# Kernel optimization log

Measured on AMD Instinct MI355X. Metric: run time of the kernel, lower is better.

## Reference

```python
import jax, jax.numpy as jnp
import numpy as np

EPS = 1e-4          # scn.BatchNormLeakyReLU default eps
LEAKINESS = 0.333   # scn.BatchNormLeakyReLU default leakiness
Z, Y, X = 3, 1280, 2048
N_ACTIVE = 1_500_000
CIN, COUT = 32, 64
KVOL = 4  # filter [1,2,2]


def setup_inputs() -> dict:
    key = jax.random.key(0)
    k1, k2, k3 = jax.random.split(key, 3)
    rng = np.random.default_rng(0)
    flat = rng.choice(Z * Y * X, size=N_ACTIVE, replace=False)
    z = flat // (Y * X)
    rem = flat % (Y * X)
    y = rem // X
    x = rem % X
    # stride==filter_size [1,2,2]: each input hits exactly one output site / offset
    out_flat = z * ((Y // 2) * (X // 2)) + (y // 2) * (X // 2) + (x // 2)
    uniq, inv = np.unique(out_flat, return_inverse=True)
    out_idx = jnp.asarray(inv.astype(np.int32))
    kern_idx = jnp.asarray(((y % 2) * 2 + (x % 2)).astype(np.int32))
    n_out = int(uniq.shape[0])
    features = jax.random.normal(k1, (N_ACTIVE, CIN), dtype=jnp.float32)
    weight = jax.random.normal(k2, (KVOL, CIN, COUT), dtype=jnp.float32) * np.float32(
        np.sqrt(2.0 / (KVOL * CIN)))
    bias = jax.random.normal(k3, (COUT,), dtype=jnp.float32) * 0.01
    gamma = jnp.ones((COUT,), dtype=jnp.float32)
    beta = jnp.zeros((COUT,), dtype=jnp.float32)
    return {"features": features, "weight": weight, "bias": bias,
            "gamma": gamma, "beta": beta, "out_idx": out_idx,
            "kern_idx": kern_idx, "n_out": n_out}


def reference(features, weight, bias, gamma, beta, out_idx, kern_idx, n_out):
    # --- sparse conv: rulebook gather-GEMM-scatter -----------------------
    out = jnp.zeros((n_out, weight.shape[-1]), dtype=features.dtype)
    for k in range(weight.shape[0]):  # fixed kernel volume = 4
        masked = jnp.where((kern_idx == k)[:, None], features, 0.0)
        out = out + jax.ops.segment_sum(masked @ weight[k], out_idx,
                                        num_segments=n_out)
    out = out + bias
    # --- fused BatchNorm (training stats over active sites) + LeakyReLU --
    mean = jnp.mean(out, axis=0)
    var = jnp.mean(jnp.square(out - mean), axis=0)  # biased, as BN
    y = gamma * (out - mean) * jax.lax.rsqrt(var + EPS) + beta
    return jnp.where(y > 0, y, LEAKINESS * y)
```

## Files before the change

### kernel.cpp

```cpp
#include <hip/hip_runtime.h>

#define LEAK 0.333f
#define BN_EPS 1e-4f

typedef __fp16 h2 __attribute__((ext_vector_type(2)));
typedef __fp16 h8 __attribute__((ext_vector_type(8)));
typedef float  f4 __attribute__((ext_vector_type(4)));

union H8 { h2 p[4]; h8 v; };

__global__ __launch_bounds__(256) void fill_table_kernel(
    const int* __restrict__ out_idx, const int* __restrict__ kern_idx,
    int* __restrict__ table, int n_in)
{
    const int i = blockIdx.x * 256 + threadIdx.x;
    if (i < n_in) {
        table[out_idx[i] * 4 + kern_idx[i]] = i;
    }
}

__global__ __launch_bounds__(256, 2) void gather_conv_kernel(
    const float* __restrict__ feat, const float* __restrict__ weight,
    const int4* __restrict__ table, float* __restrict__ out,
    float* __restrict__ stats, int n_out)
{
    const int lane = threadIdx.x & 63;
    const int wv   = threadIdx.x >> 6;
    const int c    = lane & 15;
    const int g    = lane >> 4;
    const int g8   = g * 8;

    H8 bw[4][4];
#pragma unroll
    for (int s = 0; s < 4; ++s)
#pragma unroll
        for (int n = 0; n < 4; ++n)
#pragma unroll
            for (int e = 0; e < 4; ++e) {
                const int k0 = g8 + 2 * e;
                bw[s][n].p[e] = __builtin_amdgcn_cvt_pkrtz(
                    weight[(s * 32 + k0    ) * 64 + n * 16 + c],
                    weight[(s * 32 + k0 + 1) * 64 + n * 16 + c]);
            }

    float sv[4] = {0.f, 0.f, 0.f, 0.f};
    float qv[4] = {0.f, 0.f, 0.f, 0.f};

    const int ntiles  = (n_out + 15) >> 4;
    const int tstride = gridDim.x * 4;
    int t = blockIdx.x * 4 + wv;

    int4 sl = make_int4(-1, -1, -1, -1);
    if (t < ntiles) {
        const int row = t * 16 + c;
        if (row < n_out) sl = table[row];
    }

    for (; t < ntiles; t += tstride) {
        const int tn = t + tstride;
        int4 sln = make_int4(-1, -1, -1, -1);
        if (tn < ntiles) {
            const int rown = tn * 16 + c;
            if (rown < n_out) sln = table[rown];
        }

        f4 va[4][2];
#pragma unroll
        for (int s = 0; s < 4; ++s) { va[s][0] = 0.f; va[s][1] = 0.f; }
        const int si[4] = {sl.x, sl.y, sl.z, sl.w};
#pragma unroll
        for (int s = 0; s < 4; ++s) {
            if (si[s] >= 0) {
                const float* p = feat + (size_t)si[s] * 32 + g8;
                va[s][0] = *(const f4*)p;
                va[s][1] = *(const f4*)(p + 4);
            }
        }

        H8 af[4];
#pragma unroll
        for (int s = 0; s < 4; ++s) {
            af[s].p[0] = __builtin_amdgcn_cvt_pkrtz(va[s][0].x, va[s][0].y);
            af[s].p[1] = __builtin_amdgcn_cvt_pkrtz(va[s][0].z, va[s][0].w);
            af[s].p[2] = __builtin_amdgcn_cvt_pkrtz(va[s][1].x, va[s][1].y);
            af[s].p[3] = __builtin_amdgcn_cvt_pkrtz(va[s][1].z, va[s][1].w);
        }

        f4 acc[4];
#pragma unroll
        for (int n = 0; n < 4; ++n) acc[n] = 0.f;
#pragma unroll
        for (int s = 0; s < 4; ++s)
#pragma unroll
            for (int n = 0; n < 4; ++n)
                acc[n] = __builtin_amdgcn_mfma_f32_16x16x32_f16(
                    af[s].v, bw[s][n].v, acc[n], 0, 0, 0);

        const int rbase = t * 16 + g * 4;
#pragma unroll
        for (int r = 0; r < 4; ++r) {
            const int ro = rbase + r;
            if (ro < n_out) {
                float* po = out + (size_t)ro * 64 + c;
#pragma unroll
                for (int n = 0; n < 4; ++n) po[n * 16] = acc[n][r];
            }
#pragma unroll
            for (int n = 0; n < 4; ++n) {
                sv[n] += acc[n][r];
                qv[n] = fmaf(acc[n][r], acc[n][r], qv[n]);
            }
        }
        sl = sln;
    }

#pragma unroll
    for (int n = 0; n < 4; ++n) {
        sv[n] += __shfl_xor(sv[n], 16);
        sv[n] += __shfl_xor(sv[n], 32);
        qv[n] += __shfl_xor(qv[n], 16);
        qv[n] += __shfl_xor(qv[n], 32);
    }

    __shared__ float ls[4][64];
    __shared__ float lq[4][64];
    if (lane < 16) {
#pragma unroll
        for (int n = 0; n < 4; ++n) {
            ls[wv][n * 16 + lane] = sv[n];
            lq[wv][n * 16 + lane] = qv[n];
        }
    }
    __syncthreads();
    if (wv == 0) {
        float ts = ls[0][lane] + ls[1][lane] + ls[2][lane] + ls[3][lane];
        float tq = lq[0][lane] + lq[1][lane] + lq[2][lane] + lq[3][lane];
        atomicAdd(&stats[lane], ts);
        atomicAdd(&stats[64 + lane], tq);
    }
}

__global__ void finalize_kernel(float* __restrict__ stats,
                                const float* __restrict__ gamma,
                                const float* __restrict__ beta, float inv_n)
{
    const int j = threadIdx.x;
    float mean = stats[j] * inv_n;
    float var  = fmaf(-mean, mean, stats[64 + j] * inv_n);
    var = fmaxf(var, 0.f);
    float scale = gamma[j] * rsqrtf(var + BN_EPS);
    stats[128 + j] = scale;
    stats[192 + j] = beta[j] - mean * scale;
}

__global__ __launch_bounds__(256) void apply_kernel(
    float* __restrict__ out, const float* __restrict__ stats, int n4)
{
    __shared__ float sscale[64];
    __shared__ float sshift[64];
    if (threadIdx.x < 64) {
        sscale[threadIdx.x] = stats[128 + threadIdx.x];
        sshift[threadIdx.x] = stats[192 + threadIdx.x];
    }
    __syncthreads();
    const int idx = blockIdx.x * blockDim.x + threadIdx.x;
    const int stride = gridDim.x * blockDim.x;
    float4* o4 = (float4*)out;
    for (int i = idx; i < n4; i += stride) {
        const int cb = (i * 4) & 63;
        float4 v = o4[i];
        v.x = fmaf(v.x, sscale[cb + 0], sshift[cb + 0]);
        v.y = fmaf(v.y, sscale[cb + 1], sshift[cb + 1]);
        v.z = fmaf(v.z, sscale[cb + 2], sshift[cb + 2]);
        v.w = fmaf(v.w, sscale[cb + 3], sshift[cb + 3]);
        v.x = v.x > 0.f ? v.x : LEAK * v.x;
        v.y = v.y > 0.f ? v.y : LEAK * v.y;
        v.z = v.z > 0.f ? v.z : LEAK * v.z;
        v.w = v.w > 0.f ? v.w : LEAK * v.w;
        o4[i] = v;
    }
}

extern "C" void kernel_launch(void* const* d_in, const int* in_sizes, int n_in,
                              void* d_out, int out_size, void* d_ws, size_t ws_size,
                              hipStream_t stream)
{
    const float* feat     = (const float*)d_in[0];
    const float* weight   = (const float*)d_in[1];
    const float* gamma    = (const float*)d_in[3];
    const float* beta     = (const float*)d_in[4];
    const int*   out_idx  = (const int*)d_in[5];
    const int*   kern_idx = (const int*)d_in[6];
    const int n_active = in_sizes[5];
    const int n_out    = out_size / 64;
    float* out   = (float*)d_out;
    float* stats = (float*)d_ws;
    int*   table = (int*)((char*)d_ws + 1024);

    (void)hipMemsetAsync(stats, 0, 512, stream);
    (void)hipMemsetAsync(table, 0xFF, (size_t)n_out * 4 * sizeof(int), stream);

    fill_table_kernel<<<(n_active + 255) / 256, 256, 0, stream>>>(
        out_idx, kern_idx, table, n_active);
    gather_conv_kernel<<<2048, 256, 0, stream>>>(
        feat, weight, (const int4*)table, out, stats, n_out);
    finalize_kernel<<<1, 64, 0, stream>>>(stats, gamma, beta, 1.0f / (float)n_out);
    apply_kernel<<<2048, 256, 0, stream>>>(out, stats, out_size / 4);
}
```

Baseline: 584.6 us.

## Recompute sparse conv in second pass with fused BN+LeakyReLU epilogue

Splits the conv into a stats-only pass and a second pass that recomputes the gather-GEMM and applies BatchNorm scale/shift plus LeakyReLU before storing. This removes the fp32 intermediate output write plus the separate read-modify-write apply pass, in exchange for gathering the features twice. It also software-pipelines the feature gather one tile ahead in registers, which may raise register pressure.

```diff
diff --git a/kernel.cpp b/kernel.cpp
--- a/kernel.cpp
+++ b/kernel.cpp
@@ -19,7 +19,8 @@
     }
 }
 
-__global__ __launch_bounds__(256, 2) void gather_conv_kernel(
+template <bool APPLY>
+__global__ __launch_bounds__(256, 2) void conv_pass_kernel(
     const float* __restrict__ feat, const float* __restrict__ weight,
     const int4* __restrict__ table, float* __restrict__ out,
     float* __restrict__ stats, int n_out)
@@ -43,6 +44,15 @@
                     weight[(s * 32 + k0 + 1) * 64 + n * 16 + c]);
             }
 
+    float scl[4], sft[4];
+    if (APPLY) {
+#pragma unroll
+        for (int n = 0; n < 4; ++n) {
+            scl[n] = stats[128 + n * 16 + c];
+            sft[n] = stats[192 + n * 16 + c];
+        }
+    }
+
     float sv[4] = {0.f, 0.f, 0.f, 0.f};
     float qv[4] = {0.f, 0.f, 0.f, 0.f};
 
@@ -50,30 +60,53 @@
     const int tstride = gridDim.x * 4;
     int t = blockIdx.x * 4 + wv;
 
-    int4 sl = make_int4(-1, -1, -1, -1);
+    int4 sl  = make_int4(-1, -1, -1, -1);
+    int4 sl1 = make_int4(-1, -1, -1, -1);
+    f4 va[4][2];
+#pragma unroll
+    for (int s = 0; s < 4; ++s) { va[s][0] = 0.f; va[s][1] = 0.f; }
+
     if (t < ntiles) {
         const int row = t * 16 + c;
         if (row < n_out) sl = table[row];
+        const int si0[4] = {sl.x, sl.y, sl.z, sl.w};
+#pragma unroll
+        for (int s = 0; s < 4; ++s) {
+            if (si0[s] >= 0) {
+                const float* p = feat + (size_t)si0[s] * 32 + g8;
+                va[s][0] = *(const f4*)p;
+                va[s][1] = *(const f4*)(p + 4);
+            }
+        }
+        const int tn = t + tstride;
+        if (tn < ntiles) {
+            const int rn = tn * 16 + c;
+            if (rn < n_out) sl1 = table[rn];
+        }
     }
 
     for (; t < ntiles; t += tstride) {
         const int tn = t + tstride;
-        int4 sln = make_int4(-1, -1, -1, -1);
+
+        int4 sl2 = make_int4(-1, -1, -1, -1);
+        const int tn2 = tn + tstride;
+        if (tn2 < ntiles) {
+            const int rn2 = tn2 * 16 + c;
+            if (rn2 < n_out) sl2 = table[rn2];
+        }
+
+        f4 vb[4][2];
+#pragma unroll
+        for (int s = 0; s < 4; ++s) { vb[s][0] = 0.f; vb[s][1] = 0.f; }
         if (tn < ntiles) {
-            const int rown = tn * 16 + c;
-            if (rown < n_out) sln = table[rown];
-        }
-
-        f4 va[4][2];
-#pragma unroll
-        for (int s = 0; s < 4; ++s) { va[s][0] = 0.f; va[s][1] = 0.f; }
-        const int si[4] = {sl.x, sl.y, sl.z, sl.w};
-#pragma unroll
-        for (int s = 0; s < 4; ++s) {
-            if (si[s] >= 0) {
-                const float* p = feat + (size_t)si[s] * 32 + g8;
-                va[s][0] = *(const f4*)p;
-                va[s][1] = *(const f4*)(p + 4);
+            const int si1[4] = {sl1.x, sl1.y, sl1.z, sl1.w};
+#pragma unroll
+            for (int s = 0; s < 4; ++s) {
+                if (si1[s] >= 0) {
+                    const float* p = feat + (size_t)si1[s] * 32 + g8;
+                    vb[s][0] = *(const f4*)p;
+                    vb[s][1] = *(const f4*)(p + 4);
+                }
             }
         }
 
@@ -100,43 +133,54 @@
 #pragma unroll
         for (int r = 0; r < 4; ++r) {
             const int ro = rbase + r;
-            if (ro < n_out) {
-                float* po = out + (size_t)ro * 64 + c;
-#pragma unroll
-                for (int n = 0; n < 4; ++n) po[n * 16] = acc[n][r];
-            }
+            if (APPLY) {
+                if (ro < n_out) {
+                    float* po = out + (size_t)ro * 64 + c;
+#pragma unroll
+                    for (int n = 0; n < 4; ++n) {
+                        float y = fmaf(acc[n][r], scl[n], sft[n]);
+                        po[n * 16] = y > 0.f ? y : LEAK * y;
+                    }
+                }
+            } else {
+#pragma unroll
+                for (int n = 0; n < 4; ++n) {
+                    sv[n] += acc[n][r];
+                    qv[n] = fmaf(acc[n][r], acc[n][r], qv[n]);
+                }
+            }
+        }
+
+#pragma unroll
+        for (int s = 0; s < 4; ++s) { va[s][0] = vb[s][0]; va[s][1] = vb[s][1]; }
+        sl1 = sl2;
+    }
+
+    if constexpr (!APPLY) {
+#pragma unroll
+        for (int n = 0; n < 4; ++n) {
+            sv[n] += __shfl_xor(sv[n], 16);
+            sv[n] += __shfl_xor(sv[n], 32);
+            qv[n] += __shfl_xor(qv[n], 16);
+            qv[n] += __shfl_xor(qv[n], 32);
+        }
+
+        __shared__ float ls[4][64];
+        __shared__ float lq[4][64];
+        if (lane < 16) {
 #pragma unroll
             for (int n = 0; n < 4; ++n) {
-                sv[n] += acc[n][r];
-                qv[n] = fmaf(acc[n][r], acc[n][r], qv[n]);
-            }
-        }
-        sl = sln;
-    }
-
-#pragma unroll
-    for (int n = 0; n < 4; ++n) {
-        sv[n] += __shfl_xor(sv[n], 16);
-        sv[n] += __shfl_xor(sv[n], 32);
-        qv[n] += __shfl_xor(qv[n], 16);
-        qv[n] += __shfl_xor(qv[n], 32);
-    }
-
-    __shared__ float ls[4][64];
-    __shared__ float lq[4][64];
-    if (lane < 16) {
-#pragma unroll
-        for (int n = 0; n < 4; ++n) {
-            ls[wv][n * 16 + lane] = sv[n];
-            lq[wv][n * 16 + lane] = qv[n];
-        }
-    }
-    __syncthreads();
-    if (wv == 0) {
-        float ts = ls[0][lane] + ls[1][lane] + ls[2][lane] + ls[3][lane];
-        float tq = lq[0][lane] + lq[1][lane] + lq[2][lane] + lq[3][lane];
-        atomicAdd(&stats[lane], ts);
-        atomicAdd(&stats[64 + lane], tq);
+                ls[wv][n * 16 + lane] = sv[n];
+                lq[wv][n * 16 + lane] = qv[n];
+            }
+        }
+        __syncthreads();
+        if (wv == 0) {
+            float ts = ls[0][lane] + ls[1][lane] + ls[2][lane] + ls[3][lane];
+            float tq = lq[0][lane] + lq[1][lane] + lq[2][lane] + lq[3][lane];
+            atomicAdd(&stats[lane], ts);
+            atomicAdd(&stats[64 + lane], tq);
+        }
     }
 }
 
@@ -151,34 +195,6 @@
     float scale = gamma[j] * rsqrtf(var + BN_EPS);
     stats[128 + j] = scale;
     stats[192 + j] = beta[j] - mean * scale;
-}
-
-__global__ __launch_bounds__(256) void apply_kernel(
-    float* __restrict__ out, const float* __restrict__ stats, int n4)
-{
-    __shared__ float sscale[64];
-    __shared__ float sshift[64];
-    if (threadIdx.x < 64) {
-        sscale[threadIdx.x] = stats[128 + threadIdx.x];
-        sshift[threadIdx.x] = stats[192 + threadIdx.x];
-    }
-    __syncthreads();
-    const int idx = blockIdx.x * blockDim.x + threadIdx.x;
-    const int stride = gridDim.x * blockDim.x;
-    float4* o4 = (float4*)out;
-    for (int i = idx; i < n4; i += stride) {
-        const int cb = (i * 4) & 63;
-        float4 v = o4[i];
-        v.x = fmaf(v.x, sscale[cb + 0], sshift[cb + 0]);
-        v.y = fmaf(v.y, sscale[cb + 1], sshift[cb + 1]);
-        v.z = fmaf(v.z, sscale[cb + 2], sshift[cb + 2]);
-        v.w = fmaf(v.w, sscale[cb + 3], sshift[cb + 3]);
-        v.x = v.x > 0.f ? v.x : LEAK * v.x;
-        v.y = v.y > 0.f ? v.y : LEAK * v.y;
-        v.z = v.z > 0.f ? v.z : LEAK * v.z;
-        v.w = v.w > 0.f ? v.w : LEAK * v.w;
-        o4[i] = v;
-    }
 }
 
 extern "C" void kernel_launch(void* const* d_in, const int* in_sizes, int n_in,
@@ -202,8 +218,9 @@
 
     fill_table_kernel<<<(n_active + 255) / 256, 256, 0, stream>>>(
         out_idx, kern_idx, table, n_active);
-    gather_conv_kernel<<<2048, 256, 0, stream>>>(
+    conv_pass_kernel<false><<<2048, 256, 0, stream>>>(
+        feat, weight, (const int4*)table, nullptr, stats, n_out);
+    finalize_kernel<<<1, 64, 0, stream>>>(stats, gamma, beta, 1.0f / (float)n_out);
+    conv_pass_kernel<true><<<2048, 256, 0, stream>>>(
         feat, weight, (const int4*)table, out, stats, n_out);
-    finalize_kernel<<<1, 64, 0, stream>>>(stats, gamma, beta, 1.0f / (float)n_out);
-    apply_kernel<<<2048, 256, 0, stream>>>(out, stats, out_size / 4);
-}
+}
```

Result: faster. 549.4 us (-6.0%).
